# Optimization experiments

Hardware: AMD Instinct MI355X
Metric: run time of the kernel (lower is better)

The kernel has to match this reference:

```python
import jax, jax.numpy as jnp
import numpy as np
import math

B, S, HID, NH, HD = 8, 1024, 1024, 16, 64
MAX_REL = 64

def _sinusoid_table(n_position, d_hid):
    pos = np.arange(n_position)[:, None].astype(np.float64)
    i = np.arange(d_hid)[None, :]
    angle = pos / np.power(10000.0, 2.0 * (i // 2) / d_hid)
    table = np.where(i % 2 == 0, np.sin(angle), np.cos(angle))
    return table.astype(np.float32)

def _relative_table():
    # NEZHA google-style relative position embeddings, frozen sinusoid
    dist = np.arange(S)[None, :] - np.arange(S)[:, None]
    idx = np.clip(dist, -MAX_REL, MAX_REL) + MAX_REL  # [S,S] in [0, 2*MAX_REL]
    table = _sinusoid_table(2 * MAX_REL + 1, HD)
    return jnp.asarray(table[idx])  # [S,S,HD]

def setup_inputs() -> dict:
    key = jax.random.key(0)
    ks = jax.random.split(key, 6)
    std = 0.02
    return {
        'hidden_states': jax.random.normal(ks[0], (B, S, HID), jnp.float32),
        'Wq': jax.random.normal(ks[1], (HID, HID), jnp.float32) * std,
        'bq': jnp.zeros((HID,), jnp.float32),
        'Wk': jax.random.normal(ks[2], (HID, HID), jnp.float32) * std,
        'bk': jnp.zeros((HID,), jnp.float32),
        'Wv': jax.random.normal(ks[3], (HID, HID), jnp.float32) * std,
        'bv': jnp.zeros((HID,), jnp.float32),
        'Wo': jax.random.normal(ks[4], (HID, HID), jnp.float32) * std,
        'bo': jnp.zeros((HID,), jnp.float32),
        'rel': _relative_table(),
    }

def reference(hidden_states, Wq, bq, Wk, bk, Wv, bv, Wo, bo, rel):
    b, s, _ = hidden_states.shape
    def heads(x):
        return x.reshape(b, s, NH, HD).transpose(0, 2, 1, 3)  # [B,NH,S,HD]
    q = heads(hidden_states @ Wq.T + bq)
    k = heads(hidden_states @ Wk.T + bk)
    v = heads(hidden_states @ Wv.T + bv)
    # content scores + relative-key scores (NEZHA typical_relative)
    scores = jnp.einsum('bnih,bnjh->bnij', q, k)
    scores = scores + jnp.einsum('bnih,ijh->bnij', q, rel)
    scores = scores / math.sqrt(HD)  # attention_scale=True
    probs = jax.nn.softmax(scores, axis=-1)  # dropout inactive (eval)
    ctx = jnp.einsum('bnij,bnjh->bnih', probs, v)
    ctx = ctx + jnp.einsum('bnij,ijh->bnih', probs, rel)  # relative-value term
    ctx = ctx.transpose(0, 2, 1, 3).reshape(b, s, NH * HD)
    return ctx @ Wo.T + bo
```

## Files before the change

### kernel.cpp

```cpp
#include <hip/hip_runtime.h>
#include <hip/hip_bf16.h>
#include <stdint.h>

#define SEQ 1024

typedef unsigned short u16;
typedef __attribute__((ext_vector_type(8))) short short8;
typedef __attribute__((ext_vector_type(4))) float f32x4;

static __device__ __forceinline__ u16 f2bf(float f) {
  union { float f; unsigned int u; } v; v.f = f;
  unsigned int u = v.u;
  unsigned int r = u + 0x7fffu + ((u >> 16) & 1u);
  return (u16)(r >> 16);
}
static __device__ __forceinline__ float bf2f(u16 h) {
  union { unsigned int u; float f; } v; v.u = ((unsigned int)h) << 16;
  return v.f;
}

typedef __attribute__((address_space(3))) uint32_t lds_u32;
typedef const __attribute__((address_space(1))) uint32_t glb_u32;
static __device__ __forceinline__ void gload_lds16(const void* g, void* l) {
  __builtin_amdgcn_global_load_lds((glb_u32*)(uintptr_t)g, (lds_u32*)(uintptr_t)l, 16, 0, 0);
}

__global__ __launch_bounds__(256) void cvt_f32_bf16(const float* __restrict__ src,
                                                    u16* __restrict__ dst, int n) {
  int i = (blockIdx.x * 256 + threadIdx.x) * 4;
  if (i < n) {
    float4 v = *(const float4*)(src + i);
    ushort4 o;
    o.x = f2bf(v.x); o.y = f2bf(v.y); o.z = f2bf(v.z); o.w = f2bf(v.w);
    *(ushort4*)(dst + i) = o;
  }
}

template<int OUTF32>
__global__ __launch_bounds__(256) void gemm_bt(const u16* __restrict__ A,
                                               const u16* __restrict__ Bw,
                                               const float* __restrict__ bias,
                                               void* __restrict__ Cout,
                                               int M, int N, int K) {
  const int tid  = threadIdx.x;
  const int lane = tid & 63;
  const int w    = tid >> 6;
  const int g    = lane >> 4;
  const int li   = lane & 15;
  const int m0 = blockIdx.y * 128;
  const int n0 = blockIdx.x * 128;
  const int wm = (w >> 1) * 64;
  const int wn = (w & 1) * 64;

  __shared__ alignas(16) u16 As[2][128 * 32];
  __shared__ alignas(16) u16 Bs[2][128 * 32];

  f32x4 acc[4][4];
#pragma unroll
  for (int mt = 0; mt < 4; ++mt)
#pragma unroll
    for (int nt = 0; nt < 4; ++nt) acc[mt][nt] = (f32x4){0.f, 0.f, 0.f, 0.f};

  const int KT = K >> 5;

  auto issue = [&](int t, int bb) {
#pragma unroll
    for (int c = 0; c < 2; ++c) {
      int u   = c * 256 + tid;
      int row = u >> 2, col = (u & 3) * 8;
      const u16* ga = A  + (size_t)(m0 + row) * K + t * 32 + col;
      const u16* gb = Bw + (size_t)(n0 + row) * K + t * 32 + col;
      u16* la = &As[bb][(c * 256 + w * 64) * 8];
      u16* lb = &Bs[bb][(c * 256 + w * 64) * 8];
      gload_lds16(ga, la);
      gload_lds16(gb, lb);
    }
  };

  issue(0, 0);
  for (int t = 0; t < KT; ++t) {
    __syncthreads();
    if (t + 1 < KT) issue(t + 1, (t + 1) & 1);
    const u16* as = As[t & 1];
    const u16* bs = Bs[t & 1];
    short8 af[4], bfr[4];
#pragma unroll
    for (int mt = 0; mt < 4; ++mt)
      af[mt] = *(const short8*)(&as[(wm + mt * 16 + li) * 32 + g * 8]);
#pragma unroll
    for (int nt = 0; nt < 4; ++nt)
      bfr[nt] = *(const short8*)(&bs[(wn + nt * 16 + li) * 32 + g * 8]);
#pragma unroll
    for (int mt = 0; mt < 4; ++mt)
#pragma unroll
      for (int nt = 0; nt < 4; ++nt)
        acc[mt][nt] = __builtin_amdgcn_mfma_f32_16x16x32_bf16(af[mt], bfr[nt], acc[mt][nt], 0, 0, 0);
  }

#pragma unroll
  for (int mt = 0; mt < 4; ++mt) {
#pragma unroll
    for (int nt = 0; nt < 4; ++nt) {
      int col = n0 + wn + nt * 16 + li;
      float bv = bias[col];
#pragma unroll
      for (int r = 0; r < 4; ++r) {
        int row = m0 + wm + mt * 16 + g * 4 + r;
        float v = acc[mt][nt][r] + bv;
        if (OUTF32) ((float*)Cout)[(size_t)row * N + col] = v;
        else        ((u16*)Cout)[(size_t)row * N + col]   = f2bf(v);
      }
    }
  }
}

__global__ __launch_bounds__(256) void transpose_v(const u16* __restrict__ Vb,
                                                   u16* __restrict__ Vt) {
  const int tid = threadIdx.x;
  const int bh = blockIdx.x >> 3;
  const int jt = blockIdx.x & 7;
  const int b  = bh >> 4, h = bh & 15;
  const int j0 = jt * 128;
  __shared__ alignas(16) u16 Ls[128][64];

#pragma unroll
  for (int c = 0; c < 4; ++c) {
    int flat = c * 256 + tid;
    int j = flat >> 3, hd8 = flat & 7;
    int ch = hd8 ^ ((j >> 3) & 7);
    *(uint4*)(&Ls[j][ch * 8]) =
        *(const uint4*)(Vb + (size_t)(b * SEQ + j0 + j) * 1024 + h * 64 + hd8 * 8);
  }
  __syncthreads();
#pragma unroll
  for (int c = 0; c < 4; ++c) {
    int flat = c * 256 + tid;
    int hd = flat >> 4, jj = (flat & 15) * 8;
    int cx = ((hd >> 3) ^ ((jj >> 3) & 7)) * 8 + (hd & 7);
    u16 tmp[8];
#pragma unroll
    for (int e = 0; e < 8; ++e) tmp[e] = Ls[jj + e][cx];
    *(uint4*)(Vt + (size_t)(bh * 64 + hd) * SEQ + j0 + jj) = *(uint4*)tmp;
  }
}

__global__ __launch_bounds__(256) void attn_kernel(const u16* __restrict__ Qb,
                                                   const u16* __restrict__ Kb,
                                                   const u16* __restrict__ Vt,
                                                   const float* __restrict__ rel,
                                                   u16* __restrict__ Cb) {
  const int tid  = threadIdx.x;
  const int lane = tid & 63;
  const int w    = tid >> 6;
  const int g    = lane >> 4;
  const int li   = lane & 15;

  const int bh = blockIdx.x >> 4;
  const int it = blockIdx.x & 15;
  const int b  = bh >> 4;
  const int h  = bh & 15;
  const int i0 = it * 64;

  union SU {
    struct { u16 Ks[64][72]; u16 Vs[64][72]; u16 Ps[64][72]; } m;
    struct { u16 Tn[144][72]; } i;
    struct { u16 Tt[64][160]; } e;
  };
  __shared__ alignas(16) SU su;
  __shared__ alignas(16) u16 Qr[64][132];
  __shared__ alignas(16) u16 Bd[64][160];

#pragma unroll
  for (int c = 0; c < 36; ++c) {
    int flat = c * 256 + tid;
    int d = flat >> 6, hh = flat & 63;
    float v = (d <= 128) ? rel[((size_t)(512 * 1024 + 448 + d)) * 64 + hh] : 0.f;
    su.i.Tn[d][hh] = f2bf(v);
  }
#pragma unroll
  for (int c = 0; c < 20; ++c)
    ((uint32_t*)Bd)[c * 256 + tid] = 0u;

  const size_t qrow = ((size_t)(b * SEQ + i0 + 16 * w + li)) * 1024 + h * 64;
  short8 aq[2];
  aq[0] = *(const short8*)(Qb + qrow + g * 8);
  aq[1] = *(const short8*)(Qb + qrow + 32 + g * 8);
  __syncthreads();

  {
    f32x4 qa[9];
#pragma unroll
    for (int nt = 0; nt < 9; ++nt) qa[nt] = (f32x4){0.f, 0.f, 0.f, 0.f};
#pragma unroll
    for (int kk = 0; kk < 2; ++kk)
#pragma unroll
      for (int nt = 0; nt < 9; ++nt) {
        short8 bt = *(const short8*)(&su.i.Tn[nt * 16 + li][kk * 32 + g * 8]);
        qa[nt] = __builtin_amdgcn_mfma_f32_16x16x32_bf16(aq[kk], bt, qa[nt], 0, 0, 0);
      }
#pragma unroll
    for (int nt = 0; nt < 9; ++nt) {
      int d = nt * 16 + li;
      if (d <= 128) {
#pragma unroll
        for (int r = 0; r < 4; ++r)
          Qr[16 * w + g * 4 + r][d] = f2bf(qa[nt][r]);
      }
    }
  }
  __syncthreads();

  f32x4 cacc[4];
#pragma unroll
  for (int nt = 0; nt < 4; ++nt) cacc[nt] = (f32x4){0.f, 0.f, 0.f, 0.f};
  float tsum[4] = {0.f, 0.f, 0.f, 0.f};
  float lsum[4] = {0.f, 0.f, 0.f, 0.f};
  float rsum[4] = {0.f, 0.f, 0.f, 0.f};

  const size_t kbase = ((size_t)(b * SEQ)) * 1024 + h * 64;
  const size_t vbase = ((size_t)bh) * 64 * SEQ;

  for (int t = 0; t < 16; ++t) {
    const int j0 = t * 64;
#pragma unroll
    for (int c = 0; c < 2; ++c) {
      int uu = c * 256 + tid;
      int row = uu >> 3, col = (uu & 7) * 8;
      *(uint4*)(&su.m.Ks[row][col]) =
          *(const uint4*)(Kb + kbase + (size_t)(j0 + row) * 1024 + col);
      *(uint4*)(&su.m.Vs[row][col]) =
          *(const uint4*)(Vt + vbase + (size_t)row * SEQ + j0 + col);
    }
    __syncthreads();

    f32x4 sa[4];
#pragma unroll
    for (int nt = 0; nt < 4; ++nt) sa[nt] = (f32x4){0.f, 0.f, 0.f, 0.f};
#pragma unroll
    for (int kk = 0; kk < 2; ++kk)
#pragma unroll
      for (int nt = 0; nt < 4; ++nt) {
        short8 bk = *(const short8*)(&su.m.Ks[nt * 16 + li][kk * 32 + g * 8]);
        sa[nt] = __builtin_amdgcn_mfma_f32_16x16x32_bf16(aq[kk], bk, sa[nt], 0, 0, 0);
      }

#pragma unroll
    for (int nt = 0; nt < 4; ++nt) {
      int jl = nt * 16 + li;
      int jg = j0 + jl;
#pragma unroll
      for (int r = 0; r < 4; ++r) {
        int il = 16 * w + g * 4 + r;
        int ig = i0 + il;
        int dist = jg - ig;
        int d = dist < -64 ? 0 : (dist > 64 ? 128 : dist + 64);
        float p = exp2f((sa[nt][r] + bf2f(Qr[il][d])) * 0.18033688011112042f);
        su.m.Ps[il][jl] = f2bf(p);
        tsum[r] += p;
        if (dist <= -64)      lsum[r] += p;
        else if (dist >= 64)  rsum[r] += p;
        else                  Bd[il][dist + 64] = f2bf(p);
      }
    }
    __syncthreads();

#pragma unroll
    for (int kt = 0; kt < 2; ++kt) {
      short8 pa = *(const short8*)(&su.m.Ps[16 * w + li][kt * 32 + g * 8]);
#pragma unroll
      for (int nt = 0; nt < 4; ++nt) {
        short8 bv = *(const short8*)(&su.m.Vs[nt * 16 + li][kt * 32 + g * 8]);
        cacc[nt] = __builtin_amdgcn_mfma_f32_16x16x32_bf16(pa, bv, cacc[nt], 0, 0, 0);
      }
    }
    __syncthreads();
  }

#pragma unroll
  for (int r = 0; r < 4; ++r) {
#pragma unroll
    for (int m = 1; m < 16; m <<= 1) {
      tsum[r] += __shfl_xor(tsum[r], m, 16);
      lsum[r] += __shfl_xor(lsum[r], m, 16);
      rsum[r] += __shfl_xor(rsum[r], m, 16);
    }
  }
  if (li == 0) {
#pragma unroll
    for (int r = 0; r < 4; ++r) {
      Bd[16 * w + g * 4 + r][0]   = f2bf(lsum[r]);
      Bd[16 * w + g * 4 + r][128] = f2bf(rsum[r]);
    }
  }
#pragma unroll
  for (int c = 0; c < 40; ++c) {
    int flat = c * 256 + tid;
    int d = flat >> 6, hh = flat & 63;
    float v = (d <= 128) ? rel[((size_t)(512 * 1024 + 448 + d)) * 64 + hh] : 0.f;
    su.e.Tt[hh][d] = f2bf(v);
  }
  __syncthreads();

#pragma unroll
  for (int kt = 0; kt < 5; ++kt) {
    short8 pa = *(const short8*)(&Bd[16 * w + li][kt * 32 + g * 8]);
#pragma unroll
    for (int nt = 0; nt < 4; ++nt) {
      short8 bv = *(const short8*)(&su.e.Tt[nt * 16 + li][kt * 32 + g * 8]);
      cacc[nt] = __builtin_amdgcn_mfma_f32_16x16x32_bf16(pa, bv, cacc[nt], 0, 0, 0);
    }
  }

  const size_t obase = ((size_t)(b * SEQ + i0)) * 1024 + h * 64;
#pragma unroll
  for (int r = 0; r < 4; ++r) {
    float inv = 1.f / tsum[r];
    int il = 16 * w + g * 4 + r;
#pragma unroll
    for (int nt = 0; nt < 4; ++nt)
      Cb[obase + (size_t)il * 1024 + nt * 16 + li] = f2bf(cacc[nt][r] * inv);
  }
}

extern "C" void kernel_launch(void* const* d_in, const int* in_sizes, int n_in,
                              void* d_out, int out_size, void* d_ws, size_t ws_size,
                              hipStream_t stream) {
  const float* H   = (const float*)d_in[0];
  const float* Wq  = (const float*)d_in[1];
  const float* bq  = (const float*)d_in[2];
  const float* Wk  = (const float*)d_in[3];
  const float* bk  = (const float*)d_in[4];
  const float* Wv  = (const float*)d_in[5];
  const float* bv  = (const float*)d_in[6];
  const float* Wo  = (const float*)d_in[7];
  const float* bo  = (const float*)d_in[8];
  const float* rel = (const float*)d_in[9];
  float* out = (float*)d_out;

  char* ws = (char*)d_ws;
  u16* Hb  = (u16*)(ws);
  u16* Wqb = (u16*)(ws + 16777216);
  u16* Wkb = (u16*)(ws + 18874368);
  u16* Wvb = (u16*)(ws + 20971520);
  u16* Wob = (u16*)(ws + 23068672);
  u16* Qb  = (u16*)(ws + 25165824);
  u16* Kb  = (u16*)(ws + 41943040);
  u16* Vb  = (u16*)(ws + 58720256);
  u16* Cb  = (u16*)(ws + 75497472);
  u16* Vtb = Hb;

  cvt_f32_bf16<<<8192, 256, 0, stream>>>(H,  Hb,  8388608);
  cvt_f32_bf16<<<1024, 256, 0, stream>>>(Wq, Wqb, 1048576);
  cvt_f32_bf16<<<1024, 256, 0, stream>>>(Wk, Wkb, 1048576);
  cvt_f32_bf16<<<1024, 256, 0, stream>>>(Wv, Wvb, 1048576);
  cvt_f32_bf16<<<1024, 256, 0, stream>>>(Wo, Wob, 1048576);

  dim3 gg(8, 64);
  gemm_bt<0><<<gg, 256, 0, stream>>>(Hb, Wqb, bq, Qb, 8192, 1024, 1024);
  gemm_bt<0><<<gg, 256, 0, stream>>>(Hb, Wkb, bk, Kb, 8192, 1024, 1024);
  gemm_bt<0><<<gg, 256, 0, stream>>>(Hb, Wvb, bv, Vb, 8192, 1024, 1024);

  transpose_v<<<1024, 256, 0, stream>>>(Vb, Vtb);

  attn_kernel<<<2048, 256, 0, stream>>>(Qb, Kb, Vtb, rel, Cb);

  gemm_bt<1><<<gg, 256, 0, stream>>>(Cb, Wob, bo, out, 8192, 1024, 1024);
}
```

Baseline: 664.5 us.

## Fuse Q/K/V projections into one GEMM with transposed V epilogue

Concatenates the Wq/Wk/Wv weights into one buffer and runs a single 24x64-block GEMM instead of three launches. The V slice is written already transposed into the per-head layout the attention kernel expects, which removes the separate transpose_v kernel and its extra pass over V. The tail reduction of the attention kernel is also moved after the rel-table load so they share one barrier. The V epilogue now does strided 8-byte scattered stores, which may coalesce worse than the old row-major writes.

```diff
diff --git a/kernel.cpp b/kernel.cpp
--- a/kernel.cpp
+++ b/kernel.cpp
@@ -36,12 +36,11 @@
   }
 }
 
-template<int OUTF32>
-__global__ __launch_bounds__(256) void gemm_bt(const u16* __restrict__ A,
-                                               const u16* __restrict__ Bw,
-                                               const float* __restrict__ bias,
-                                               void* __restrict__ Cout,
-                                               int M, int N, int K) {
+__global__ __launch_bounds__(256) void gemm_out(const u16* __restrict__ A,
+                                                const u16* __restrict__ Bw,
+                                                const float* __restrict__ bias,
+                                                float* __restrict__ Cout,
+                                                int M, int N, int K) {
   const int tid  = threadIdx.x;
   const int lane = tid & 63;
   const int w    = tid >> 6;
@@ -106,41 +105,109 @@
 #pragma unroll
       for (int r = 0; r < 4; ++r) {
         int row = m0 + wm + mt * 16 + g * 4 + r;
-        float v = acc[mt][nt][r] + bv;
-        if (OUTF32) ((float*)Cout)[(size_t)row * N + col] = v;
-        else        ((u16*)Cout)[(size_t)row * N + col]   = f2bf(v);
-      }
-    }
-  }
-}
-
-__global__ __launch_bounds__(256) void transpose_v(const u16* __restrict__ Vb,
-                                                   u16* __restrict__ Vt) {
-  const int tid = threadIdx.x;
-  const int bh = blockIdx.x >> 3;
-  const int jt = blockIdx.x & 7;
-  const int b  = bh >> 4, h = bh & 15;
-  const int j0 = jt * 128;
-  __shared__ alignas(16) u16 Ls[128][64];
-
-#pragma unroll
-  for (int c = 0; c < 4; ++c) {
-    int flat = c * 256 + tid;
-    int j = flat >> 3, hd8 = flat & 7;
-    int ch = hd8 ^ ((j >> 3) & 7);
-    *(uint4*)(&Ls[j][ch * 8]) =
-        *(const uint4*)(Vb + (size_t)(b * SEQ + j0 + j) * 1024 + h * 64 + hd8 * 8);
-  }
-  __syncthreads();
-#pragma unroll
-  for (int c = 0; c < 4; ++c) {
-    int flat = c * 256 + tid;
-    int hd = flat >> 4, jj = (flat & 15) * 8;
-    int cx = ((hd >> 3) ^ ((jj >> 3) & 7)) * 8 + (hd & 7);
-    u16 tmp[8];
-#pragma unroll
-    for (int e = 0; e < 8; ++e) tmp[e] = Ls[jj + e][cx];
-    *(uint4*)(Vt + (size_t)(bh * 64 + hd) * SEQ + j0 + jj) = *(uint4*)tmp;
+        Cout[(size_t)row * N + col] = acc[mt][nt][r] + bv;
+      }
+    }
+  }
+}
+
+__global__ __launch_bounds__(256) void gemm_qkv(const u16* __restrict__ A,
+                                                const u16* __restrict__ Wc,
+                                                const float* __restrict__ bq,
+                                                const float* __restrict__ bk,
+                                                const float* __restrict__ bv,
+                                                u16* __restrict__ Qb,
+                                                u16* __restrict__ Kb,
+                                                u16* __restrict__ Vtb) {
+  const int tid  = threadIdx.x;
+  const int lane = tid & 63;
+  const int w    = tid >> 6;
+  const int g    = lane >> 4;
+  const int li   = lane & 15;
+  const int m0 = blockIdx.y * 128;
+  const int n0 = blockIdx.x * 128;
+  const int wm = (w >> 1) * 64;
+  const int wn = (w & 1) * 64;
+  const int K = 1024;
+
+  __shared__ alignas(16) u16 As[2][128 * 32];
+  __shared__ alignas(16) u16 Bs[2][128 * 32];
+
+  f32x4 acc[4][4];
+#pragma unroll
+  for (int mt = 0; mt < 4; ++mt)
+#pragma unroll
+    for (int nt = 0; nt < 4; ++nt) acc[mt][nt] = (f32x4){0.f, 0.f, 0.f, 0.f};
+
+  auto issue = [&](int t, int bb) {
+#pragma unroll
+    for (int c = 0; c < 2; ++c) {
+      int u   = c * 256 + tid;
+      int row = u >> 2, col = (u & 3) * 8;
+      const u16* ga = A  + (size_t)(m0 + row) * K + t * 32 + col;
+      const u16* gb = Wc + (size_t)(n0 + row) * K + t * 32 + col;
+      u16* la = &As[bb][(c * 256 + w * 64) * 8];
+      u16* lb = &Bs[bb][(c * 256 + w * 64) * 8];
+      gload_lds16(ga, la);
+      gload_lds16(gb, lb);
+    }
+  };
+
+  issue(0, 0);
+  for (int t = 0; t < 32; ++t) {
+    __syncthreads();
+    if (t + 1 < 32) issue(t + 1, (t + 1) & 1);
+    const u16* as = As[t & 1];
+    const u16* bs = Bs[t & 1];
+    short8 af[4], bfr[4];
+#pragma unroll
+    for (int mt = 0; mt < 4; ++mt)
+      af[mt] = *(const short8*)(&as[(wm + mt * 16 + li) * 32 + g * 8]);
+#pragma unroll
+    for (int nt = 0; nt < 4; ++nt)
+      bfr[nt] = *(const short8*)(&bs[(wn + nt * 16 + li) * 32 + g * 8]);
+#pragma unroll
+    for (int mt = 0; mt < 4; ++mt)
+#pragma unroll
+      for (int nt = 0; nt < 4; ++nt)
+        acc[mt][nt] = __builtin_amdgcn_mfma_f32_16x16x32_bf16(af[mt], bfr[nt], acc[mt][nt], 0, 0, 0);
+  }
+
+  const int mat = n0 >> 10;
+  if (mat < 2) {
+    u16* dst = mat ? Kb : Qb;
+    const float* bp = mat ? bk : bq;
+    const int cb = n0 & 1023;
+#pragma unroll
+    for (int mt = 0; mt < 4; ++mt) {
+#pragma unroll
+      for (int nt = 0; nt < 4; ++nt) {
+        int col = cb + wn + nt * 16 + li;
+        float bvv = bp[col];
+#pragma unroll
+        for (int r = 0; r < 4; ++r) {
+          int row = m0 + wm + mt * 16 + g * 4 + r;
+          dst[(size_t)row * 1024 + col] = f2bf(acc[mt][nt][r] + bvv);
+        }
+      }
+    }
+  } else {
+#pragma unroll
+    for (int mt = 0; mt < 4; ++mt) {
+#pragma unroll
+      for (int nt = 0; nt < 4; ++nt) {
+        int ncol = (n0 & 1023) + wn + nt * 16 + li;
+        float bvv = bv[ncol];
+        int mbase = m0 + wm + mt * 16 + g * 4;
+        size_t vrow = ((size_t)((mbase >> 10) * 16 + (ncol >> 6))) * 64 + (ncol & 63);
+        ushort4 pk;
+        pk.x = f2bf(acc[mt][nt][0] + bvv);
+        pk.y = f2bf(acc[mt][nt][1] + bvv);
+        pk.z = f2bf(acc[mt][nt][2] + bvv);
+        pk.w = f2bf(acc[mt][nt][3] + bvv);
+        *(ushort4*)(Vtb + vrow * 1024 + (mbase & 1023)) = pk;
+      }
+    }
   }
 }
 
@@ -218,7 +285,7 @@
   float rsum[4] = {0.f, 0.f, 0.f, 0.f};
 
   const size_t kbase = ((size_t)(b * SEQ)) * 1024 + h * 64;
-  const size_t vbase = ((size_t)bh) * 64 * SEQ;
+  const size_t vbase = ((size_t)bh) * 64 * 1024;
 
   for (int t = 0; t < 16; ++t) {
     const int j0 = t * 64;
@@ -269,29 +336,13 @@
       short8 pa = *(const short8*)(&su.m.Ps[16 * w + li][kt * 32 + g * 8]);
 #pragma unroll
       for (int nt = 0; nt < 4; ++nt) {
-        short8 bv = *(const short8*)(&su.m.Vs[nt * 16 + li][kt * 32 + g * 8]);
-        cacc[nt] = __builtin_amdgcn_mfma_f32_16x16x32_bf16(pa, bv, cacc[nt], 0, 0, 0);
+        short8 bvv = *(const short8*)(&su.m.Vs[nt * 16 + li][kt * 32 + g * 8]);
+        cacc[nt] = __builtin_amdgcn_mfma_f32_16x16x32_bf16(pa, bvv, cacc[nt], 0, 0, 0);
       }
     }
     __syncthreads();
   }
 
-#pragma unroll
-  for (int r = 0; r < 4; ++r) {
-#pragma unroll
-    for (int m = 1; m < 16; m <<= 1) {
-      tsum[r] += __shfl_xor(tsum[r], m, 16);
-      lsum[r] += __shfl_xor(lsum[r], m, 16);
-      rsum[r] += __shfl_xor(rsum[r], m, 16);
-    }
-  }
-  if (li == 0) {
-#pragma unroll
-    for (int r = 0; r < 4; ++r) {
-      Bd[16 * w + g * 4 + r][0]   = f2bf(lsum[r]);
-      Bd[16 * w + g * 4 + r][128] = f2bf(rsum[r]);
-    }
-  }
 #pragma unroll
   for (int c = 0; c < 40; ++c) {
     int flat = c * 256 + tid;
@@ -299,6 +350,24 @@
     float v = (d <= 128) ? rel[((size_t)(512 * 1024 + 448 + d)) * 64 + hh] : 0.f;
     su.e.Tt[hh][d] = f2bf(v);
   }
+
+#pragma unroll
+  for (int r = 0; r < 4; ++r) {
+#pragma unroll
+    for (int m = 1; m < 16; m <<= 1) {
+      tsum[r] += __shfl_xor(tsum[r], m, 16);
+      lsum[r] += __shfl_xor(lsum[r], m, 16);
+      rsum[r] += __shfl_xor(rsum[r], m, 16);
+    }
+  }
+  if (li == 0) {
+#pragma unroll
+    for (int r = 0; r < 4; ++r) {
+      int il = 16 * w + g * 4 + r;
+      Bd[il][0]   = f2bf(lsum[r]);
+      Bd[il][128] = f2bf(rsum[r]);
+    }
+  }
   __syncthreads();
 
 #pragma unroll
@@ -306,8 +375,8 @@
     short8 pa = *(const short8*)(&Bd[16 * w + li][kt * 32 + g * 8]);
 #pragma unroll
     for (int nt = 0; nt < 4; ++nt) {
-      short8 bv = *(const short8*)(&su.e.Tt[nt * 16 + li][kt * 32 + g * 8]);
-      cacc[nt] = __builtin_amdgcn_mfma_f32_16x16x32_bf16(pa, bv, cacc[nt], 0, 0, 0);
+      short8 bvv = *(const short8*)(&su.e.Tt[nt * 16 + li][kt * 32 + g * 8]);
+      cacc[nt] = __builtin_amdgcn_mfma_f32_16x16x32_bf16(pa, bvv, cacc[nt], 0, 0, 0);
     }
   }
 
@@ -338,31 +407,23 @@
   float* out = (float*)d_out;
 
   char* ws = (char*)d_ws;
-  u16* Hb  = (u16*)(ws);
-  u16* Wqb = (u16*)(ws + 16777216);
-  u16* Wkb = (u16*)(ws + 18874368);
-  u16* Wvb = (u16*)(ws + 20971520);
-  u16* Wob = (u16*)(ws + 23068672);
-  u16* Qb  = (u16*)(ws + 25165824);
-  u16* Kb  = (u16*)(ws + 41943040);
-  u16* Vb  = (u16*)(ws + 58720256);
-  u16* Cb  = (u16*)(ws + 75497472);
-  u16* Vtb = Hb;
+  u16* Hb   = (u16*)(ws);
+  u16* Wcat = (u16*)(ws + 16777216);
+  u16* Wob  = (u16*)(ws + 23068672);
+  u16* Qb   = (u16*)(ws + 25165824);
+  u16* Kb   = (u16*)(ws + 41943040);
+  u16* Vtb  = (u16*)(ws + 58720256);
+  u16* Cb   = (u16*)(ws + 75497472);
 
   cvt_f32_bf16<<<8192, 256, 0, stream>>>(H,  Hb,  8388608);
-  cvt_f32_bf16<<<1024, 256, 0, stream>>>(Wq, Wqb, 1048576);
-  cvt_f32_bf16<<<1024, 256, 0, stream>>>(Wk, Wkb, 1048576);
-  cvt_f32_bf16<<<1024, 256, 0, stream>>>(Wv, Wvb, 1048576);
+  cvt_f32_bf16<<<1024, 256, 0, stream>>>(Wq, Wcat,           1048576);
+  cvt_f32_bf16<<<1024, 256, 0, stream>>>(Wk, Wcat + 1048576, 1048576);
+  cvt_f32_bf16<<<1024, 256, 0, stream>>>(Wv, Wcat + 2097152, 1048576);
   cvt_f32_bf16<<<1024, 256, 0, stream>>>(Wo, Wob, 1048576);
 
-  dim3 gg(8, 64);
-  gemm_bt<0><<<gg, 256, 0, stream>>>(Hb, Wqb, bq, Qb, 8192, 1024, 1024);
-  gemm_bt<0><<<gg, 256, 0, stream>>>(Hb, Wkb, bk, Kb, 8192, 1024, 1024);
-  gemm_bt<0><<<gg, 256, 0, stream>>>(Hb, Wvb, bv, Vb, 8192, 1024, 1024);
-
-  transpose_v<<<1024, 256, 0, stream>>>(Vb, Vtb);
+  gemm_qkv<<<dim3(24, 64), 256, 0, stream>>>(Hb, Wcat, bq, bk, bv, Qb, Kb, Vtb);
 
   attn_kernel<<<2048, 256, 0, stream>>>(Qb, Kb, Vtb, rel, Cb);
 
-  gemm_bt<1><<<gg, 256, 0, stream>>>(Cb, Wob, bo, out, 8192, 1024, 1024);
-}
+  gemm_out<<<dim3(8, 64), 256, 0, stream>>>(Cb, Wob, bo, out, 8192, 1024, 1024);
+}
```

Result: faster. 650.4 us (-2.1%).
